# Performance work log

Hardware: AMD Instinct MI355X
Metric: run time of the kernel (lower is better)

Reference implementation:

```python
import jax, jax.numpy as jnp
import numpy as np

N_NODES = 100000
N_EDGES = 3200000
IN_DIM = 128
H1, F1 = 8, 8          # layer1: 8 heads x 8 feats -> concat 64
N_CLASSES = 40         # layer2: 1 head -> classes
NEG_SLOPE = 0.2        # GAT LeakyReLU slope


def setup_inputs() -> dict:
    key = jax.random.key(0)
    ks = jax.random.split(key, 8)
    x = jax.random.normal(ks[0], (N_NODES, IN_DIM), dtype=jnp.float32)
    adj = jax.random.randint(ks[1], (2, N_EDGES), 0, N_NODES, dtype=jnp.int64)
    s1 = 1.0 / np.sqrt(IN_DIM)
    s2 = 1.0 / np.sqrt(H1 * F1)
    W1 = jax.random.normal(ks[2], (IN_DIM, H1 * F1), dtype=jnp.float32) * s1
    a1_src = jax.random.normal(ks[3], (H1, F1), dtype=jnp.float32) * s2
    a1_dst = jax.random.normal(ks[4], (H1, F1), dtype=jnp.float32) * s2
    W2 = jax.random.normal(ks[5], (H1 * F1, N_CLASSES), dtype=jnp.float32) * s2
    a2_src = jax.random.normal(ks[6], (1, N_CLASSES), dtype=jnp.float32) * s2
    a2_dst = jax.random.normal(ks[7], (1, N_CLASSES), dtype=jnp.float32) * s2
    return {"input_matrix": x, "adjacency_coo_matrix": adj,
            "W1": W1, "a1_src": a1_src, "a1_dst": a1_dst,
            "W2": W2, "a2_src": a2_src, "a2_dst": a2_dst}


def gat_layer(x, src, dst, W, a_s, a_d, heads, fdim):
    n = x.shape[0]
    h = (x @ W).reshape(n, heads, fdim)                 # [N,H,F]
    e_src = jnp.sum(h * a_s, axis=-1)                   # [N,H]
    e_dst = jnp.sum(h * a_d, axis=-1)                   # [N,H]
    e = jax.nn.leaky_relu(e_src[src] + e_dst[dst], NEG_SLOPE)  # [E,H]
    m = jax.ops.segment_max(e, dst, num_segments=n)     # per-dst softmax max
    p = jnp.exp(e - m[dst])
    s = jax.ops.segment_sum(p, dst, num_segments=n)
    alpha = p / s[dst]                                  # [E,H]
    out = jax.ops.segment_sum(alpha[:, :, None] * h[src], dst, num_segments=n)
    return out                                          # [N,H,F]


def reference(input_matrix, adjacency_coo_matrix, W1, a1_src, a1_dst, W2, a2_src, a2_dst):
    n = input_matrix.shape[0]
    loops = jnp.arange(n, dtype=adjacency_coo_matrix.dtype)
    src = jnp.concatenate([adjacency_coo_matrix[0], loops])
    dst = jnp.concatenate([adjacency_coo_matrix[1], loops])
    x = gat_layer(input_matrix, src, dst, W1, a1_src, a1_dst, H1, F1)
    x = jax.nn.elu(x.reshape(n, H1 * F1))               # concat heads + ELU
    x = gat_layer(x, src, dst, W2, a2_src, a2_dst, 1, N_CLASSES)
    return jax.nn.log_softmax(x.reshape(n, N_CLASSES), axis=1)
```

## Files before the change

### kernel.cpp

```cpp
#include <hip/hip_runtime.h>
#include <hip/hip_fp16.h>
#include <math.h>

#define NN 100000
#define EE 3200000
#define ET (EE + NN)
#define BKW 128
#define NBK ((NN + BKW - 1) / BKW)
#define BCAP 5120
#define EPB 4096
#define NB_P1 ((EE + EPB - 1) / EPB)
#define NB_G 391

typedef float v2f __attribute__((ext_vector_type(2)));
typedef float v4f __attribute__((ext_vector_type(4)));
typedef _Float16 v8h __attribute__((ext_vector_type(8)));

__device__ __forceinline__ float lrelu(float v) { return fmaxf(v, 0.2f * v); }

__device__ __forceinline__ unsigned char to_fp8(float v) {
  return (unsigned char)(__builtin_amdgcn_cvt_pk_fp8_f32(v, v, 0, false) & 0xff);
}


__global__ __launch_bounds__(256) void k_p1(
    const int* __restrict__ srcs, const int* __restrict__ dsts,
    int* __restrict__ bcount, int* __restrict__ bbuf) {
  __shared__ int lcnt[NBK];
  __shared__ int lbase[NBK];
  int tid = threadIdx.x;
  for (int i = tid; i < NBK; i += 256) lcnt[i] = 0;
  __syncthreads();
  int rem = EE - blockIdx.x * EPB;
  bool valid = (tid * 16) < rem;
  int e0 = blockIdx.x * EPB + tid * 16;
  int rank[16], bkt[16], pk[16];
  if (valid) {
    const int4* dp = reinterpret_cast<const int4*>(dsts + e0);
    const int4* sp = reinterpret_cast<const int4*>(srcs + e0);
    int4 d4[4], s4[4];
#pragma unroll
    for (int i = 0; i < 4; ++i) { d4[i] = dp[i]; s4[i] = sp[i]; }
#pragma unroll
    for (int i = 0; i < 16; ++i) {
      int d = ((const int*)d4)[i];
      int s = ((const int*)s4)[i];
      int b = d >> 7;
      rank[i] = atomicAdd(&lcnt[b], 1);
      bkt[i] = b;
      pk[i] = (s << 7) | (d & 127);
    }
  }
  __syncthreads();
  for (int i = tid; i < NBK; i += 256) {
    int c = lcnt[i];
    lbase[i] = c ? atomicAdd(&bcount[i], c) : 0;
  }
  __syncthreads();
  if (valid) {
#pragma unroll
    for (int i = 0; i < 16; ++i)
      bbuf[(size_t)bkt[i] * BCAP + lbase[bkt[i]] + rank[i]] = pk[i];
  }
}


__global__ __launch_bounds__(256) void k_g1(
    const float* __restrict__ x, const float* __restrict__ W1,
    const float* __restrict__ a1d,
    unsigned char* __restrict__ P1, __half* __restrict__ ed1) {
  __shared__ _Float16 Wb[16 * 64 * 8];
  int tid = threadIdx.x;
  int gbid = blockIdx.x;
  for (int idx = tid; idx < 16 * 64; idx += 256) {
    int f = idx >> 6, l = idx & 63;
    int nt = f >> 2, kk = f & 3;
    int ql = l >> 4, cl = l & 15;
    int col = nt * 16 + cl;
    int k0 = kk * 32 + ql * 8;
    v8h tmp;
#pragma unroll
    for (int j = 0; j < 8; ++j) tmp[j] = (_Float16)W1[(k0 + j) * 64 + col];
    *reinterpret_cast<v8h*>(&Wb[idx * 8]) = tmp;
  }
  __syncthreads();
  int wv = tid >> 6, lane = tid & 63;
  int q = lane >> 4, c = lane & 15;
  v8h bf[16];
#pragma unroll
  for (int f = 0; f < 16; ++f)
    bf[f] = *reinterpret_cast<const v8h*>(&Wb[(f * 64 + lane) * 8]);
  float a1d_l[4];
#pragma unroll
  for (int nt = 0; nt < 4; ++nt) a1d_l[nt] = a1d[nt * 16 + c];
  for (int t = 0; t < 4; ++t) {
    int n0 = gbid * 256 + wv * 64 + t * 16;
    int row = n0 + c;
    row = (row < NN) ? row : (NN - 1);
    v4f acc[4] = {{0.f,0.f,0.f,0.f},{0.f,0.f,0.f,0.f},{0.f,0.f,0.f,0.f},{0.f,0.f,0.f,0.f}};
#pragma unroll
    for (int kk = 0; kk < 4; ++kk) {
      const float* xp = x + (size_t)row * 128 + kk * 32 + q * 8;
      float4 x0 = *reinterpret_cast<const float4*>(xp);
      float4 x1 = *reinterpret_cast<const float4*>(xp + 4);
      v8h af;
      af[0] = (_Float16)x0.x; af[1] = (_Float16)x0.y;
      af[2] = (_Float16)x0.z; af[3] = (_Float16)x0.w;
      af[4] = (_Float16)x1.x; af[5] = (_Float16)x1.y;
      af[6] = (_Float16)x1.z; af[7] = (_Float16)x1.w;
#pragma unroll
      for (int nt = 0; nt < 4; ++nt)
        acc[nt] = __builtin_amdgcn_mfma_f32_16x16x32_f16(af, bf[nt * 4 + kk], acc[nt], 0, 0, 0);
    }
#pragma unroll
    for (int nt = 0; nt < 4; ++nt) {
#pragma unroll
      for (int r = 0; r < 4; ++r) {
        float val = acc[nt][r];
        float vd = val * a1d_l[nt];
        vd += __shfl_xor(vd, 1); vd += __shfl_xor(vd, 2); vd += __shfl_xor(vd, 4);
        int node = n0 + q * 4 + r;
        if (node < NN) {
          P1[((size_t)node << 6) + nt * 16 + c] = to_fp8(val);
          if ((c & 7) == 0) ed1[node * 8 + 2 * nt + (c >> 3)] = __float2half(vd);
        }
      }
    }
  }
}


__global__ __launch_bounds__(256) void k_p2(const int* __restrict__ bcount,
                                            const int* __restrict__ bbuf,
                                            int* __restrict__ offsets,
                                            int* __restrict__ edge_src) {
  __shared__ int cnt[BKW];
  __shared__ int s1[BKW];
  __shared__ int cur[BKW];
  __shared__ int red[256];
  __shared__ int sorted[BCAP + BKW];
  int b = blockIdx.x, tid = threadIdx.x;
  int partial = 0;
  for (int j = tid; j < b; j += 256)
    partial += bcount[j] + min(BKW, NN - (j << 7));
  red[tid] = partial;
  __syncthreads();
  for (int off = 128; off >= 1; off >>= 1) {
    if (tid < off) red[tid] += red[tid + off];
    __syncthreads();
  }
  int base = red[0];
  int d0 = b << 7;
  int width = min(BKW, NN - d0);
  int n = bcount[b];
  const int* buf = bbuf + (size_t)b * BCAP;
  if (tid < BKW) cnt[tid] = (tid < width) ? 1 : 0;
  __syncthreads();
  for (int i = tid; i < n; i += 256) atomicAdd(&cnt[buf[i] & 127], 1);
  __syncthreads();
  if (tid < BKW) s1[tid] = cnt[tid];
  __syncthreads();
  for (int off = 1; off < BKW; off <<= 1) {
    int u = (tid < BKW && tid >= off) ? s1[tid - off] : 0;
    __syncthreads();
    if (tid < BKW) s1[tid] += u;
    __syncthreads();
  }
  if (tid < width) {
    int excl = s1[tid] - cnt[tid];
    offsets[d0 + tid] = base + excl;
    sorted[excl] = d0 + tid;
    cur[tid] = excl + 1;
  }
  if (b == 0 && tid == 0) offsets[NN] = ET;
  __syncthreads();
  for (int i = tid; i < n; i += 256) {
    int p = buf[i];
    int pos = atomicAdd(&cur[p & 127], 1);
    sorted[pos] = p >> 7;
  }
  __syncthreads();
  int m = n + width;
  for (int i = tid; i < m; i += 256)
    edge_src[base + i] = sorted[i];
}


__global__ __launch_bounds__(256) void k_agg1(
    const int* __restrict__ offsets, const int* __restrict__ edge_src,
    const unsigned char* __restrict__ P1, const float* __restrict__ a1s,
    const __half* __restrict__ ed1, __half* __restrict__ x2) {
  int wv = threadIdx.x >> 6, lane = threadIdx.x & 63;
  int g = lane >> 3, p = lane & 7;
  int gbase = lane & 56;
  int dst = blockIdx.x * 32 + wv * 8 + g;
  float edv = __half2float(ed1[dst * 8 + p]);
  float4 as0 = *reinterpret_cast<const float4*>(a1s + p * 8);
  float4 as1 = *reinterpret_cast<const float4*>(a1s + p * 8 + 4);
  int beg = offsets[dst], end = offsets[dst + 1];
  int deg = end - beg;
  int md = deg;
#pragma unroll
  for (int o = 8; o < 64; o <<= 1) md = max(md, __shfl_xor(md, o, 64));
  float l = 0.f;
  float a[8] = {0.f, 0.f, 0.f, 0.f, 0.f, 0.f, 0.f, 0.f};
  for (int t = 0; t < md; t += 8) {
    int idx = t + p;
    int ci = beg + ((idx < deg) ? idx : (deg - 1));
    int mysrc = edge_src[ci];
    int src[8]; uint2 raw[8];
#pragma unroll
    for (int i = 0; i < 8; ++i) src[i] = __shfl(mysrc, gbase | i, 64);
#pragma unroll
    for (int i = 0; i < 8; ++i)
      raw[i] = *reinterpret_cast<const uint2*>(P1 + ((size_t)src[i] << 6) + (p << 3));
#pragma unroll
    for (int i = 0; i < 8; ++i) {
      v2f f01 = __builtin_amdgcn_cvt_pk_f32_fp8(raw[i].x, false);
      v2f f23 = __builtin_amdgcn_cvt_pk_f32_fp8(raw[i].x, true);
      v2f f45 = __builtin_amdgcn_cvt_pk_f32_fp8(raw[i].y, false);
      v2f f67 = __builtin_amdgcn_cvt_pk_f32_fp8(raw[i].y, true);
      float es = f01.x * as0.x + f01.y * as0.y + f23.x * as0.z + f23.y * as0.w
               + f45.x * as1.x + f45.y * as1.y + f67.x * as1.z + f67.y * as1.w;
      float e = lrelu(es + edv);
      float pr = (t + i < deg) ? __expf(e) : 0.f;
      l += pr;
      a[0] += pr * f01.x; a[1] += pr * f01.y;
      a[2] += pr * f23.x; a[3] += pr * f23.y;
      a[4] += pr * f45.x; a[5] += pr * f45.y;
      a[6] += pr * f67.x; a[7] += pr * f67.y;
    }
  }
  float rl = 1.f / l;
  union { __half h[8]; uint4 u; } pk;
#pragma unroll
  for (int i = 0; i < 8; ++i) {
    float v = a[i] * rl;
    v = (v > 0.f) ? v : (__expf(v) - 1.f);
    pk.h[i] = __float2half(v);
  }
  *reinterpret_cast<uint4*>(x2 + ((size_t)dst << 6) + (p << 3)) = pk.u;
}


__global__ __launch_bounds__(256) void k_gemm2(
    const __half* __restrict__ x2, const float* __restrict__ W2,
    const float* __restrict__ a2s, const float* __restrict__ a2d,
    unsigned char* __restrict__ P2, float* __restrict__ ed2) {
  __shared__ _Float16 Wb[6 * 64 * 8];
  int tid = threadIdx.x;
  for (int idx = tid; idx < 6 * 64; idx += 256) {
    int f = idx >> 6, l = idx & 63;
    int nt = f >> 1, kk = f & 1;
    int ql = l >> 4, cl = l & 15;
    int col = nt * 16 + cl;
    int k0 = kk * 32 + ql * 8;
    v8h tmp;
#pragma unroll
    for (int j = 0; j < 8; ++j)
      tmp[j] = (col < 40) ? (_Float16)W2[(k0 + j) * 40 + col] : (_Float16)0.f;
    *reinterpret_cast<v8h*>(&Wb[idx * 8]) = tmp;
  }
  __syncthreads();
  int wv = tid >> 6, lane = tid & 63;
  int q = lane >> 4, c = lane & 15;
  v8h bf[6];
#pragma unroll
  for (int f = 0; f < 6; ++f)
    bf[f] = *reinterpret_cast<const v8h*>(&Wb[(f * 64 + lane) * 8]);
  float a2s_l[3], a2d_l[3];
#pragma unroll
  for (int nt = 0; nt < 3; ++nt) {
    int n = nt * 16 + c;
    a2s_l[nt] = (n < 40) ? a2s[n] : 0.f;
    a2d_l[nt] = (n < 40) ? a2d[n] : 0.f;
  }
  for (int t = 0; t < 4; ++t) {
    int n0 = blockIdx.x * 256 + wv * 64 + t * 16;
    int row = n0 + c;
    row = (row < NN) ? row : (NN - 1);
    v4f acc[3] = {{0.f,0.f,0.f,0.f},{0.f,0.f,0.f,0.f},{0.f,0.f,0.f,0.f}};
#pragma unroll
    for (int kk = 0; kk < 2; ++kk) {
      v8h af = *reinterpret_cast<const v8h*>(x2 + (size_t)row * 64 + kk * 32 + q * 8);
#pragma unroll
      for (int nt = 0; nt < 3; ++nt)
        acc[nt] = __builtin_amdgcn_mfma_f32_16x16x32_f16(af, bf[nt * 2 + kk], acc[nt], 0, 0, 0);
    }
#pragma unroll
    for (int r = 0; r < 4; ++r) {
      float v0 = acc[0][r], v1 = acc[1][r], v2 = acc[2][r];
      float s = v0 * a2s_l[0] + v1 * a2s_l[1] + v2 * a2s_l[2];
      float d = v0 * a2d_l[0] + v1 * a2d_l[1] + v2 * a2d_l[2];
      s += __shfl_xor(s, 1); s += __shfl_xor(s, 2); s += __shfl_xor(s, 4); s += __shfl_xor(s, 8);
      d += __shfl_xor(d, 1); d += __shfl_xor(d, 2); d += __shfl_xor(d, 4); d += __shfl_xor(d, 8);
      int node = n0 + q * 4 + r;
      if (node < NN) {
        unsigned char* rec = P2 + ((size_t)node << 6);
        if (c < 8) rec[32 + c] = to_fp8(v2);
        rec[c]      = to_fp8(v0);
        rec[16 + c] = to_fp8(v1);
        if (c == 0) {
          *reinterpret_cast<__half*>(rec + 40) = __float2half(s);
          ed2[node] = d;
        }
      }
    }
  }
}


__global__ __launch_bounds__(256) void k_agg2(
    const int* __restrict__ offsets, const int* __restrict__ edge_src,
    const unsigned char* __restrict__ P2, const float* __restrict__ ed2,
    float* __restrict__ out) {
  int wv = threadIdx.x >> 6, lane = threadIdx.x & 63;
  int g = lane >> 3, p = lane & 7;
  bool act = p < 5;
  int cp = act ? p : 0;
  int dst = blockIdx.x * 32 + wv * 8 + g;
  float edv = ed2[dst];
  int beg = offsets[dst], end = offsets[dst + 1];
  int deg = end - beg;
  int md = deg;
#pragma unroll
  for (int o = 8; o < 64; o <<= 1) md = max(md, __shfl_xor(md, o, 64));
  int gbase = lane & 56;
  float l = 0.f;
  float a[8] = {0.f, 0.f, 0.f, 0.f, 0.f, 0.f, 0.f, 0.f};
  for (int t = 0; t < md; t += 8) {
    int idx = t + p;
    int ci = beg + ((idx < deg) ? idx : (deg - 1));
    int mysrc = edge_src[ci];
    int src[8]; uint2 raw[8];
#pragma unroll
    for (int i = 0; i < 8; ++i) src[i] = __shfl(mysrc, gbase | i, 64);
    float myes = __half2float(*reinterpret_cast<const __half*>(
        P2 + ((size_t)mysrc << 6) + 40));
    float mye = lrelu(myes + edv);
    float mypr = (t + p < deg) ? __expf(mye) : 0.f;
#pragma unroll
    for (int i = 0; i < 8; ++i)
      raw[i] = *reinterpret_cast<const uint2*>(P2 + ((size_t)src[i] << 6) + (cp << 3));
#pragma unroll
    for (int i = 0; i < 8; ++i) {
      float pr = __shfl(mypr, gbase | i, 64);
      v2f f01 = __builtin_amdgcn_cvt_pk_f32_fp8(raw[i].x, false);
      v2f f23 = __builtin_amdgcn_cvt_pk_f32_fp8(raw[i].x, true);
      v2f f45 = __builtin_amdgcn_cvt_pk_f32_fp8(raw[i].y, false);
      v2f f67 = __builtin_amdgcn_cvt_pk_f32_fp8(raw[i].y, true);
      l += pr;
      a[0] += pr * f01.x; a[1] += pr * f01.y;
      a[2] += pr * f23.x; a[3] += pr * f23.y;
      a[4] += pr * f45.x; a[5] += pr * f45.y;
      a[6] += pr * f67.x; a[7] += pr * f67.y;
    }
  }
  float rl = 1.f / l;
  float v[8];
#pragma unroll
  for (int j = 0; j < 8; ++j) v[j] = a[j] * rl;
  float red = act ? fmaxf(fmaxf(fmaxf(v[0], v[1]), fmaxf(v[2], v[3])),
                          fmaxf(fmaxf(v[4], v[5]), fmaxf(v[6], v[7])))
                  : -INFINITY;
#pragma unroll
  for (int o = 1; o < 8; o <<= 1) red = fmaxf(red, __shfl_xor(red, o, 64));
  float se = 0.f;
  if (act) {
#pragma unroll
    for (int j = 0; j < 8; ++j) se += __expf(v[j] - red);
  }
#pragma unroll
  for (int o = 1; o < 8; o <<= 1) se += __shfl_xor(se, o, 64);
  float ls = red + __logf(se);
  if (act) {
    float* op = out + (size_t)dst * 40 + (p << 3);
    *reinterpret_cast<float4*>(op) =
        make_float4(v[0] - ls, v[1] - ls, v[2] - ls, v[3] - ls);
    *reinterpret_cast<float4*>(op + 4) =
        make_float4(v[4] - ls, v[5] - ls, v[6] - ls, v[7] - ls);
  }
}


extern "C" void kernel_launch(void* const* d_in, const int* in_sizes, int n_in,
                              void* d_out, int out_size, void* d_ws, size_t ws_size,
                              hipStream_t stream) {
  const float* x   = (const float*)d_in[0];
  const int*   adj = (const int*)d_in[1];
  const float* W1  = (const float*)d_in[2];
  const float* a1s = (const float*)d_in[3];
  const float* a1d = (const float*)d_in[4];
  const float* W2  = (const float*)d_in[5];
  const float* a2s = (const float*)d_in[6];
  const float* a2d = (const float*)d_in[7];
  float* out = (float*)d_out;

  const int* srcs = adj;
  const int* dsts = adj + EE;

  char* w = (char*)d_ws;
  size_t off = 0;
  auto alloc = [&](size_t bytes) -> void* {
    void* p = w + off;
    off = (off + bytes + 255) & ~(size_t)255;
    return p;
  };
  int* offsets      = (int*)alloc((size_t)(NN + 1) * 4);
  int* edge_src     = (int*)alloc((size_t)ET * 4);
  int* bcount       = (int*)alloc((size_t)NBK * 4);
  unsigned char* P1 = (unsigned char*)alloc((size_t)NN * 64);
  __half* ed1       = (__half*)alloc((size_t)NN * 8 * 2);
  __half* x2        = (__half*)alloc((size_t)NN * 64 * 2);
  int* bbuf         = (int*)alloc((size_t)NBK * BCAP * 4);
  unsigned char* P2 = P1;
  float* ed2 = (float*)ed1;

  hipMemsetAsync(bcount, 0, (size_t)NBK * 4, stream);
  k_p1<<<NB_P1, 256, 0, stream>>>(srcs, dsts, bcount, bbuf);
  k_g1<<<NB_G, 256, 0, stream>>>(x, W1, a1d, P1, ed1);
  k_p2<<<NBK, 256, 0, stream>>>(bcount, bbuf, offsets, edge_src);

  k_agg1<<<NN / 32, 256, 0, stream>>>(offsets, edge_src, P1, a1s, ed1, x2);
  k_gemm2<<<NB_G, 256, 0, stream>>>(x2, W2, a2s, a2d, P2, ed2);
  k_agg2<<<NN / 32, 256, 0, stream>>>(offsets, edge_src, P2, ed2, out);
}
```

Baseline: 289.5 us.

## Split layer-1 aggregation into two head-half passes with planar fp8 features

Stores layer-1 projected features in two planes of 4 heads each and runs the layer-1 aggregation kernel twice, once per plane. The aim is to shrink the randomly gathered working set so gathers hit cache more often. In exchange, edge indices and offsets are read twice and there is an extra launch. Nontemporal loads and stores are also used for the edge index stream and the outputs.

```diff
diff --git a/kernel.cpp b/kernel.cpp
--- a/kernel.cpp
+++ b/kernel.cpp
@@ -11,9 +11,11 @@
 #define EPB 4096
 #define NB_P1 ((EE + EPB - 1) / EPB)
 #define NB_G 391
+#define NB_A1 ((NN + 63) / 64)
 
 typedef float v2f __attribute__((ext_vector_type(2)));
 typedef float v4f __attribute__((ext_vector_type(4)));
+typedef unsigned v4u __attribute__((ext_vector_type(4)));
 typedef _Float16 v8h __attribute__((ext_vector_type(8)));
 
 __device__ __forceinline__ float lrelu(float v) { return fmaxf(v, 0.2f * v); }
@@ -121,7 +123,8 @@
         vd += __shfl_xor(vd, 1); vd += __shfl_xor(vd, 2); vd += __shfl_xor(vd, 4);
         int node = n0 + q * 4 + r;
         if (node < NN) {
-          P1[((size_t)node << 6) + nt * 16 + c] = to_fp8(val);
+          int col = nt * 16 + c;
+          P1[((size_t)(col >> 5) * NN + node) * 32 + (col & 31)] = to_fp8(val);
           if ((c & 7) == 0) ed1[node * 8 + 2 * nt + (c >> 3)] = __float2half(vd);
         }
       }
@@ -188,34 +191,36 @@
 
 __global__ __launch_bounds__(256) void k_agg1(
     const int* __restrict__ offsets, const int* __restrict__ edge_src,
-    const unsigned char* __restrict__ P1, const float* __restrict__ a1s,
-    const __half* __restrict__ ed1, __half* __restrict__ x2) {
+    const unsigned char* __restrict__ P1h, const float* __restrict__ a1s,
+    const __half* __restrict__ ed1, __half* __restrict__ x2, int hh) {
   int wv = threadIdx.x >> 6, lane = threadIdx.x & 63;
-  int g = lane >> 3, p = lane & 7;
-  int gbase = lane & 56;
-  int dst = blockIdx.x * 32 + wv * 8 + g;
-  float edv = __half2float(ed1[dst * 8 + p]);
-  float4 as0 = *reinterpret_cast<const float4*>(a1s + p * 8);
-  float4 as1 = *reinterpret_cast<const float4*>(a1s + p * 8 + 4);
-  int beg = offsets[dst], end = offsets[dst + 1];
+  int g = lane >> 2, p = lane & 3;
+  int gbase = lane & 60;
+  int head = hh * 4 + p;
+  int dst = blockIdx.x * 64 + wv * 16 + g;
+  int dstc = (dst < NN) ? dst : (NN - 1);
+  float edv = __half2float(ed1[dstc * 8 + head]);
+  float4 as0 = *reinterpret_cast<const float4*>(a1s + head * 8);
+  float4 as1 = *reinterpret_cast<const float4*>(a1s + head * 8 + 4);
+  int beg = offsets[dstc], end = offsets[dstc + 1];
   int deg = end - beg;
   int md = deg;
 #pragma unroll
-  for (int o = 8; o < 64; o <<= 1) md = max(md, __shfl_xor(md, o, 64));
+  for (int o = 4; o < 64; o <<= 1) md = max(md, __shfl_xor(md, o, 64));
   float l = 0.f;
   float a[8] = {0.f, 0.f, 0.f, 0.f, 0.f, 0.f, 0.f, 0.f};
-  for (int t = 0; t < md; t += 8) {
+  for (int t = 0; t < md; t += 4) {
     int idx = t + p;
     int ci = beg + ((idx < deg) ? idx : (deg - 1));
-    int mysrc = edge_src[ci];
-    int src[8]; uint2 raw[8];
-#pragma unroll
-    for (int i = 0; i < 8; ++i) src[i] = __shfl(mysrc, gbase | i, 64);
-#pragma unroll
-    for (int i = 0; i < 8; ++i)
-      raw[i] = *reinterpret_cast<const uint2*>(P1 + ((size_t)src[i] << 6) + (p << 3));
-#pragma unroll
-    for (int i = 0; i < 8; ++i) {
+    int mysrc = __builtin_nontemporal_load(edge_src + ci);
+    int src[4]; uint2 raw[4];
+#pragma unroll
+    for (int i = 0; i < 4; ++i) src[i] = __shfl(mysrc, gbase | i, 64);
+#pragma unroll
+    for (int i = 0; i < 4; ++i)
+      raw[i] = *reinterpret_cast<const uint2*>(P1h + (size_t)src[i] * 32 + (p << 3));
+#pragma unroll
+    for (int i = 0; i < 4; ++i) {
       v2f f01 = __builtin_amdgcn_cvt_pk_f32_fp8(raw[i].x, false);
       v2f f23 = __builtin_amdgcn_cvt_pk_f32_fp8(raw[i].x, true);
       v2f f45 = __builtin_amdgcn_cvt_pk_f32_fp8(raw[i].y, false);
@@ -232,14 +237,16 @@
     }
   }
   float rl = 1.f / l;
-  union { __half h[8]; uint4 u; } pk;
+  union { __half h[8]; v4u u; } pk;
 #pragma unroll
   for (int i = 0; i < 8; ++i) {
     float v = a[i] * rl;
     v = (v > 0.f) ? v : (__expf(v) - 1.f);
     pk.h[i] = __float2half(v);
   }
-  *reinterpret_cast<uint4*>(x2 + ((size_t)dst << 6) + (p << 3)) = pk.u;
+  if (dst < NN)
+    __builtin_nontemporal_store(pk.u,
+        reinterpret_cast<v4u*>(x2 + ((size_t)dst << 6) + (head << 3)));
 }
 
 
@@ -331,7 +338,7 @@
   for (int t = 0; t < md; t += 8) {
     int idx = t + p;
     int ci = beg + ((idx < deg) ? idx : (deg - 1));
-    int mysrc = edge_src[ci];
+    int mysrc = __builtin_nontemporal_load(edge_src + ci);
     int src[8]; uint2 raw[8];
 #pragma unroll
     for (int i = 0; i < 8; ++i) src[i] = __shfl(mysrc, gbase | i, 64);
@@ -375,10 +382,10 @@
   float ls = red + __logf(se);
   if (act) {
     float* op = out + (size_t)dst * 40 + (p << 3);
-    *reinterpret_cast<float4*>(op) =
-        make_float4(v[0] - ls, v[1] - ls, v[2] - ls, v[3] - ls);
-    *reinterpret_cast<float4*>(op + 4) =
-        make_float4(v[4] - ls, v[5] - ls, v[6] - ls, v[7] - ls);
+    v4f o0 = {v[0] - ls, v[1] - ls, v[2] - ls, v[3] - ls};
+    v4f o1 = {v[4] - ls, v[5] - ls, v[6] - ls, v[7] - ls};
+    __builtin_nontemporal_store(o0, reinterpret_cast<v4f*>(op));
+    __builtin_nontemporal_store(o1, reinterpret_cast<v4f*>(op + 4));
   }
 }
 
@@ -421,7 +428,9 @@
   k_g1<<<NB_G, 256, 0, stream>>>(x, W1, a1d, P1, ed1);
   k_p2<<<NBK, 256, 0, stream>>>(bcount, bbuf, offsets, edge_src);
 
-  k_agg1<<<NN / 32, 256, 0, stream>>>(offsets, edge_src, P1, a1s, ed1, x2);
+  k_agg1<<<NB_A1, 256, 0, stream>>>(offsets, edge_src, P1, a1s, ed1, x2, 0);
+  k_agg1<<<NB_A1, 256, 0, stream>>>(offsets, edge_src, P1 + (size_t)NN * 32,
+                                    a1s, ed1, x2, 1);
   k_gemm2<<<NB_G, 256, 0, stream>>>(x2, W2, a2s, a2d, P2, ed2);
   k_agg2<<<NN / 32, 256, 0, stream>>>(offsets, edge_src, P2, ed2, out);
 }
```

Measured after the change: 346.8 us. +19.8%, slower.
